# Kernel optimization log

Hardware: AMD Instinct MI355X
Metric: run time of the kernel (lower is better)

## Reference

```python
import jax, jax.numpy as jnp
import numpy as np

B, S, D, H = 4, 2048, 2048, 8192  # batch, seq, d_model, hidden (power of 2 for FHT)


def fwht(x):
    """Fast Walsh-Hadamard transform along the last axis, normalized by 1/sqrt(n).

    Iterative butterfly: O(n log n). n must be a power of 2.
    """
    orig_shape = x.shape
    n = orig_shape[-1]
    x = x.reshape(-1, n)
    h = 1
    while h < n:
        # view as (rows, n/(2h) blocks, 2 halves, h) and do the butterfly
        xb = x.reshape(-1, n // (2 * h), 2, h)
        a = xb[:, :, 0, :]
        b = xb[:, :, 1, :]
        x = jnp.stack([a + b, a - b], axis=2).reshape(-1, n)
        h *= 2
    scale = jnp.asarray(1.0 / np.sqrt(n), dtype=x.dtype)
    return (x * scale).reshape(orig_shape)


def setup_inputs() -> dict:
    key = jax.random.key(0)
    kx, k1, k2, k3 = jax.random.split(key, 4)
    x = jax.random.normal(kx, (B, S, D), dtype=jnp.float32)
    # nn.Linear weights: [out_features, in_features], no bias (Llama FFN style)
    W1 = jax.random.normal(k1, (H, D), dtype=jnp.float32) * (1.0 / np.sqrt(D))
    W2 = jax.random.normal(k2, (D, H), dtype=jnp.float32) * (1.0 / np.sqrt(H))
    W3 = jax.random.normal(k3, (H, D), dtype=jnp.float32) * (1.0 / np.sqrt(D))
    return {"x": x, "W1": W1, "W2": W2, "W3": W3}


def reference(x, W1, W2, W3):
    # w2( fht( silu(w1(x)) * w3(x) ) )
    up_gate = jnp.einsum("bsd,hd->bsh", x, W1)          # w1(x): [B,S,H]
    up_lin = jnp.einsum("bsd,hd->bsh", x, W3)           # w3(x): [B,S,H]
    hidden = jax.nn.silu(up_gate) * up_lin              # SwiGLU gate
    hidden = fwht(hidden)                               # fast Hadamard transform over H
    out = jnp.einsum("bsh,dh->bsd", hidden, W2)         # w2(.): [B,S,D]
    return out
```

## Files before the change

### kernel.cpp

```cpp
#include <hip/hip_runtime.h>

typedef __attribute__((ext_vector_type(8))) __bf16 bf16x8;
typedef __attribute__((ext_vector_type(4))) float f32x4;

#define GLOAD_LDS16(g, l)                                                     \
  __builtin_amdgcn_global_load_lds(                                           \
      (const __attribute__((address_space(1))) void*)(g),                     \
      (__attribute__((address_space(3))) void*)(l), 16, 0, 0)

#define BAR() __builtin_amdgcn_s_barrier()
#define SB0() __builtin_amdgcn_sched_barrier(0)
#define LGKM(n)                                                               \
  do {                                                                        \
    asm volatile("s_waitcnt lgkmcnt(" #n ")" ::: "memory");                   \
    SB0();                                                                    \
  } while (0)
#define VMCNT0() asm volatile("s_waitcnt vmcnt(0)" ::: "memory")
#define PRIO1() __builtin_amdgcn_s_setprio(1)
#define PRIO0() __builtin_amdgcn_s_setprio(0)
#define MFMA_BF16 __builtin_amdgcn_mfma_f32_16x16x32_bf16

__device__ __forceinline__ unsigned short f32_to_bf16(float f) {
  unsigned int u = __builtin_bit_cast(unsigned int, f);
  u += 0x7FFFu + ((u >> 16) & 1u);
  return (unsigned short)(u >> 16);
}

__global__ void conv_f32_bf16(const float* __restrict__ in,
                              unsigned short* __restrict__ out, int n4) {
  int stride = gridDim.x * blockDim.x;
  for (int i = blockIdx.x * blockDim.x + threadIdx.x; i < n4; i += stride) {
    float4 v = reinterpret_cast<const float4*>(in)[i];
    ushort4 o;
    o.x = f32_to_bf16(v.x);
    o.y = f32_to_bf16(v.y);
    o.z = f32_to_bf16(v.z);
    o.w = f32_to_bf16(v.w);
    reinterpret_cast<ushort4*>(out)[i] = o;
  }
}

__global__ void fwht_rows_bf16(const float* __restrict__ in,
                               unsigned short* __restrict__ out) {
  __shared__ float s[8192];
  const int tid = threadIdx.x;
  const float* row = in + (size_t)blockIdx.x * 8192;
#pragma unroll
  for (int i = 0; i < 8; ++i)
    reinterpret_cast<float4*>(s)[tid + i * 256] =
        reinterpret_cast<const float4*>(row)[tid + i * 256];
  for (int h = 1; h < 8192; h <<= 1) {
    __syncthreads();
#pragma unroll
    for (int it = 0; it < 16; ++it) {
      int i = tid + it * 256;
      int j = ((i & ~(h - 1)) << 1) | (i & (h - 1));
      float a = s[j], b = s[j + h];
      s[j] = a + b;
      s[j + h] = a - b;
    }
  }
  __syncthreads();
  const float scale = 0.011048543456039806f;
  unsigned short* orow = out + (size_t)blockIdx.x * 8192;
#pragma unroll
  for (int i = 0; i < 8; ++i) {
    float4 v = reinterpret_cast<const float4*>(s)[tid + i * 256];
    ushort4 o;
    o.x = f32_to_bf16(v.x * scale);
    o.y = f32_to_bf16(v.y * scale);
    o.z = f32_to_bf16(v.z * scale);
    o.w = f32_to_bf16(v.w * scale);
    reinterpret_cast<ushort4*>(orow)[tid + i * 256] = o;
  }
}

#define RD_A(arr, mi, bi)                                                     \
  arr[0] = *(const bf16x8*)(Lb + ((bi)*32768 + (mi)*2048) + rA0);             \
  arr[1] = *(const bf16x8*)(Lb + ((bi)*32768 + (mi)*2048) + rA1);
#define RD_B(arr, ni, bi)                                                     \
  arr[0] = *(const bf16x8*)(Lb + ((bi)*32768 + (ni)*2048) + rB0);             \
  arr[1] = *(const bf16x8*)(Lb + ((bi)*32768 + (ni)*2048) + rB1);

#define G2_TILE(bi, tt)                                                       \
  {                                                                           \
    if ((tt) + 1 < NT) {                                                      \
      unsigned short* dA = L + (((bi) ^ 1) * 16384) + wid * 512;              \
      unsigned short* dB = L + 32768 + (((bi) ^ 1) * 16384) + wid * 512;      \
      _Pragma("unroll") for (int i = 0; i < 4; ++i) {                         \
        GLOAD_LDS16(pA + i * s64, dA + i * 4096);                             \
        GLOAD_LDS16(pB + i * s64, dB + i * 4096);                             \
      }                                                                       \
    }                                                                         \
    SB0();                                                                    \
                                       \
    RD_A(ra[0], 0, bi) RD_A(ra[1], 1, bi)                                     \
    RD_B(rb[0], 0, bi) RD_B(rb[1], 1, bi)                                     \
    SB0();                                                                    \
                                                        \
    RD_A(ra[2], 2, bi) RD_A(ra[3], 3, bi)                                     \
    SB0();                                                                    \
    LGKM(4);                                                                  \
    PRIO1();                                                                  \
    _Pragma("unroll") for (int ks = 0; ks < 2; ++ks)                          \
        _Pragma("unroll") for (int m = 0; m < 2; ++m)                         \
            _Pragma("unroll") for (int n = 0; n < 2; ++n) acc[m][n] =         \
                MFMA_BF16(ra[m][ks], rb[n][ks], acc[m][n], 0, 0, 0);          \
    PRIO0();                                                                  \
    SB0();                                                                    \
                                                        \
    RD_B(rb[2], 2, bi) RD_B(rb[3], 3, bi)                                     \
    SB0();                                                                    \
    LGKM(4);                                                                  \
    PRIO1();                                                                  \
    _Pragma("unroll") for (int ks = 0; ks < 2; ++ks)                          \
        _Pragma("unroll") for (int m = 2; m < 4; ++m)                         \
            _Pragma("unroll") for (int n = 0; n < 2; ++n) acc[m][n] =         \
                MFMA_BF16(ra[m][ks], rb[n][ks], acc[m][n], 0, 0, 0);          \
    PRIO0();                                                                  \
    SB0();                                                                    \
                                                       \
    RD_A(ra2[0], 4, bi) RD_A(ra2[1], 5, bi)                                   \
    SB0();                                                                    \
    LGKM(4);                                                                  \
    PRIO1();                                                                  \
    _Pragma("unroll") for (int ks = 0; ks < 2; ++ks)                          \
        _Pragma("unroll") for (int m = 0; m < 4; ++m)                         \
            _Pragma("unroll") for (int n = 2; n < 4; ++n) acc[m][n] =         \
                MFMA_BF16(ra[m][ks], rb[n][ks], acc[m][n], 0, 0, 0);          \
    PRIO0();                                                                  \
    SB0();                                                                    \
                                                       \
    RD_A(ra2[2], 6, bi) RD_A(ra2[3], 7, bi)                                   \
    SB0();                                                                    \
    LGKM(4);                                                                  \
    PRIO1();                                                                  \
    _Pragma("unroll") for (int ks = 0; ks < 2; ++ks)                          \
        _Pragma("unroll") for (int m = 0; m < 2; ++m)                         \
            _Pragma("unroll") for (int n = 0; n < 4; ++n) acc[4 + m][n] =     \
                MFMA_BF16(ra2[m][ks], rb[n][ks], acc[4 + m][n], 0, 0, 0);     \
    PRIO0();                                                                  \
    SB0();                                                                    \
    LGKM(0);                                                                  \
    PRIO1();                                                                  \
    _Pragma("unroll") for (int ks = 0; ks < 2; ++ks)                          \
        _Pragma("unroll") for (int m = 2; m < 4; ++m)                         \
            _Pragma("unroll") for (int n = 0; n < 4; ++n) acc[4 + m][n] =     \
                MFMA_BF16(ra2[m][ks], rb[n][ks], acc[4 + m][n], 0, 0, 0);     \
    PRIO0();                                                                  \
    VMCNT0();                                                                 \
    BAR();                                                                    \
    pA += 128;                                                                \
    pB += 128;                                                                \
  }

__launch_bounds__(512, 2)
__global__ void gemm2_pipe(const unsigned short* __restrict__ A,
                           const unsigned short* __restrict__ Bt,
                           float* __restrict__ C, int M, int N, int K) {
  __shared__ __align__(16) unsigned short L[65536];
  const int tid = threadIdx.x, lane = tid & 63, wid = tid >> 6;
  const int wr = wid >> 2, wc = wid & 3;
  const int nbx = N >> 8;
  const int cpx = (int)gridDim.x >> 3;
  const int swz = ((int)blockIdx.x & 7) * cpx + ((int)blockIdx.x >> 3);
  const int bm = (swz / nbx) << 8, bn = (swz % nbx) << 8;
  const int NT = K >> 6;

  const int lp0 = (lane & 15) * 128 + (((lane >> 4) << 4) ^ ((lane & 7) << 4));
  const int lp1 =
      (lane & 15) * 128 + ((64 | ((lane >> 4) << 4)) ^ ((lane & 7) << 4));
  const int rA0 = wr * 16384 + lp0, rA1 = wr * 16384 + lp1;
  const int rB0 = 65536 + wc * 8192 + lp0, rB1 = 65536 + wc * 8192 + lp1;

  const int swzc = ((lane & 7) ^ (lane >> 3)) << 4;
  const char* pA = (const char*)A +
                   ((size_t)(bm + (wid << 3) + (lane >> 3)) * K) * 2 + swzc;
  const char* pB = (const char*)Bt +
                   ((size_t)(bn + (wid << 3) + (lane >> 3)) * K) * 2 + swzc;
  const size_t s64 = (size_t)K * 128;
  const char* Lb = (const char*)L;

  {
    unsigned short* dA = L + wid * 512;
    unsigned short* dB = L + 32768 + wid * 512;
#pragma unroll
    for (int i = 0; i < 4; ++i) {
      GLOAD_LDS16(pA + i * s64, dA + i * 4096);
      GLOAD_LDS16(pB + i * s64, dB + i * 4096);
    }
  }
  pA += 128;
  pB += 128;

  f32x4 acc[8][4];
#pragma unroll
  for (int m = 0; m < 8; ++m)
#pragma unroll
    for (int n = 0; n < 4; ++n) acc[m][n] = (f32x4)0.0f;
  bf16x8 ra[4][2], ra2[4][2], rb[4][2];

  VMCNT0();
  BAR();

  for (int t = 0; t < NT; t += 2) {
    G2_TILE(0, t)
    G2_TILE(1, t + 1)
  }

  const int er = (lane >> 4) << 2;
  const int ec = lane & 15;
#pragma unroll
  for (int mi = 0; mi < 8; ++mi)
#pragma unroll
    for (int n = 0; n < 4; ++n)
#pragma unroll
      for (int r = 0; r < 4; ++r) {
        size_t row = (size_t)(bm + wr * 128 + mi * 16 + er + r);
        size_t col = (size_t)(bn + wc * 64 + n * 16 + ec);
        C[row * N + col] = acc[mi][n][r];
      }
}

#define RD_A1(arr, mi, bi)                                                    \
  arr[0] = *(const bf16x8*)(Lb + ((bi)*32768 + (mi)*2048) + rA0);             \
  arr[1] = *(const bf16x8*)(Lb + ((bi)*32768 + (mi)*2048) + rA1);
#define RD_B1(arr, ni, bi)                                                    \
  arr[0] = *(const bf16x8*)(Lb + (65536 + (bi)*16384 + (ni)*2048) + rBp0);    \
  arr[1] = *(const bf16x8*)(Lb + (65536 + (bi)*16384 + (ni)*2048) + rBp1);
#define RD_B3(arr, ni, bi)                                                    \
  arr[0] = *(const bf16x8*)(Lb + (98304 + (bi)*16384 + (ni)*2048) + rBp0);    \
  arr[1] = *(const bf16x8*)(Lb + (98304 + (bi)*16384 + (ni)*2048) + rBp1);

#define G1_TILE(bi, tt)                                                       \
  {                                                                           \
    if ((tt) + 1 < NT) {                                                      \
      unsigned short* dA = L + (((bi) ^ 1) * 16384) + wid * 512;              \
      unsigned short* dB1 = L + 32768 + (((bi) ^ 1) * 8192) + wid * 512;      \
      unsigned short* dB3 = L + 49152 + (((bi) ^ 1) * 8192) + wid * 512;      \
      _Pragma("unroll") for (int i = 0; i < 4; ++i)                           \
          GLOAD_LDS16(pA + i * s64, dA + i * 4096);                           \
      _Pragma("unroll") for (int i = 0; i < 2; ++i) {                         \
        GLOAD_LDS16(pB1 + i * s64, dB1 + i * 4096);                           \
        GLOAD_LDS16(pB3 + i * s64, dB3 + i * 4096);                           \
      }                                                                       \
    }                                                                         \
    SB0();                                                                    \
                                      \
    RD_A1(ra[0], 0, bi) RD_A1(ra[1], 1, bi)                                   \
    RD_B1(rb1[0], 0, bi) RD_B1(rb1[1], 1, bi)                                 \
    SB0();                                                                    \
                                                        \
    RD_A1(ra[2], 2, bi) RD_A1(ra[3], 3, bi)                                   \
    SB0();                                                                    \
    LGKM(4);                                                                  \
    PRIO1();                                                                  \
    _Pragma("unroll") for (int ks = 0; ks < 2; ++ks)                          \
        _Pragma("unroll") for (int m = 0; m < 2; ++m)                         \
            _Pragma("unroll") for (int n = 0; n < 2; ++n) accG[m][n] =        \
                MFMA_BF16(ra[m][ks], rb1[n][ks], accG[m][n], 0, 0, 0);        \
    PRIO0();                                                                  \
    SB0();                                                                    \
                                                       \
    RD_B1(rb1[2], 2, bi) RD_B1(rb1[3], 3, bi)                                 \
    SB0();                                                                    \
    LGKM(4);                                                                  \
    PRIO1();                                                                  \
    _Pragma("unroll") for (int ks = 0; ks < 2; ++ks)                          \
        _Pragma("unroll") for (int m = 2; m < 4; ++m)                         \
            _Pragma("unroll") for (int n = 0; n < 2; ++n) accG[m][n] =        \
                MFMA_BF16(ra[m][ks], rb1[n][ks], accG[m][n], 0, 0, 0);        \
    PRIO0();                                                                  \
    SB0();                                                                    \
                                                       \
    RD_B3(rb3[2], 2, bi) RD_B3(rb3[3], 3, bi)                                 \
    SB0();                                                                    \
    LGKM(4);                                                                  \
    PRIO1();                                                                  \
    _Pragma("unroll") for (int ks = 0; ks < 2; ++ks)                          \
        _Pragma("unroll") for (int m = 0; m < 4; ++m)                         \
            _Pragma("unroll") for (int n = 2; n < 4; ++n) accG[m][n] =        \
                MFMA_BF16(ra[m][ks], rb1[n][ks], accG[m][n], 0, 0, 0);        \
    PRIO0();                                                                  \
    SB0();                                                                    \
                                                       \
    RD_B3(rb3[0], 0, bi) RD_B3(rb3[1], 1, bi)                                 \
    SB0();                                                                    \
    LGKM(4);                                                                  \
    PRIO1();                                                                  \
    _Pragma("unroll") for (int ks = 0; ks < 2; ++ks)                          \
        _Pragma("unroll") for (int m = 0; m < 4; ++m)                         \
            _Pragma("unroll") for (int n = 2; n < 4; ++n) accL[m][n] =        \
                MFMA_BF16(ra[m][ks], rb3[n][ks], accL[m][n], 0, 0, 0);        \
    PRIO0();                                                                  \
    SB0();                                                                    \
    LGKM(0);                                                                  \
    PRIO1();                                                                  \
    _Pragma("unroll") for (int ks = 0; ks < 2; ++ks)                          \
        _Pragma("unroll") for (int m = 0; m < 4; ++m)                         \
            _Pragma("unroll") for (int n = 0; n < 2; ++n) accL[m][n] =        \
                MFMA_BF16(ra[m][ks], rb3[n][ks], accL[m][n], 0, 0, 0);        \
    PRIO0();                                                                  \
    VMCNT0();                                                                 \
    BAR();                                                                    \
    pA += 128;                                                                \
    pB1 += 128;                                                               \
    pB3 += 128;                                                               \
  }

__launch_bounds__(512, 2)
__global__ void gemm1_pipe(const unsigned short* __restrict__ A,
                           const unsigned short* __restrict__ B1p,
                           const unsigned short* __restrict__ B3p,
                           unsigned short* __restrict__ Hout, int M, int N,
                           int K) {
  __shared__ __align__(16) unsigned short L[65536];
  const int tid = threadIdx.x, lane = tid & 63, wid = tid >> 6;
  const int wr = wid >> 1, wc = wid & 1;
  const int nby = M >> 8;
  const int cpx = (int)gridDim.x >> 3;
  const int swz = ((int)blockIdx.x & 7) * cpx + ((int)blockIdx.x >> 3);
  const int bm = (swz % nby) << 8;
  const int bn = (swz / nby) << 7;
  const int NT = K >> 6;

  const int lp0 = (lane & 15) * 128 + (((lane >> 4) << 4) ^ ((lane & 7) << 4));
  const int lp1 =
      (lane & 15) * 128 + ((64 | ((lane >> 4) << 4)) ^ ((lane & 7) << 4));
  const int rA0 = wr * 8192 + lp0, rA1 = wr * 8192 + lp1;
  const int rBp0 = wc * 8192 + lp0, rBp1 = wc * 8192 + lp1;

  const int swzc = ((lane & 7) ^ (lane >> 3)) << 4;
  const char* pA = (const char*)A +
                   ((size_t)(bm + (wid << 3) + (lane >> 3)) * K) * 2 + swzc;
  const char* pB1 = (const char*)B1p +
                    ((size_t)(bn + (wid << 3) + (lane >> 3)) * K) * 2 + swzc;
  const char* pB3 = (const char*)B3p +
                    ((size_t)(bn + (wid << 3) + (lane >> 3)) * K) * 2 + swzc;
  const size_t s64 = (size_t)K * 128;
  const char* Lb = (const char*)L;

  {
    unsigned short* dA = L + wid * 512;
    unsigned short* dB1 = L + 32768 + wid * 512;
    unsigned short* dB3 = L + 49152 + wid * 512;
#pragma unroll
    for (int i = 0; i < 4; ++i) GLOAD_LDS16(pA + i * s64, dA + i * 4096);
#pragma unroll
    for (int i = 0; i < 2; ++i) {
      GLOAD_LDS16(pB1 + i * s64, dB1 + i * 4096);
      GLOAD_LDS16(pB3 + i * s64, dB3 + i * 4096);
    }
  }
  pA += 128;
  pB1 += 128;
  pB3 += 128;

  f32x4 accG[4][4], accL[4][4];
#pragma unroll
  for (int m = 0; m < 4; ++m)
#pragma unroll
    for (int n = 0; n < 4; ++n) {
      accG[m][n] = (f32x4)0.0f;
      accL[m][n] = (f32x4)0.0f;
    }
  bf16x8 ra[4][2], rb1[4][2], rb3[4][2];

  VMCNT0();
  BAR();

  for (int t = 0; t < NT; t += 2) {
    G1_TILE(0, t)
    G1_TILE(1, t + 1)
  }

  const int er = (lane >> 4) << 2;
  const int ec = lane & 15;
#pragma unroll
  for (int m = 0; m < 4; ++m)
#pragma unroll
    for (int n = 0; n < 4; ++n)
#pragma unroll
      for (int r = 0; r < 4; ++r) {
        float g = accG[m][n][r];
        float li = accL[m][n][r];
        float h = (g / (1.0f + __expf(-g))) * li;
        size_t row = (size_t)(bm + wr * 64 + m * 16 + er + r);
        size_t col = (size_t)(bn + wc * 64 + n * 16 + ec);
        Hout[row * N + col] = f32_to_bf16(h);
      }
}

extern "C" void kernel_launch(void* const* d_in, const int* in_sizes, int n_in,
                              void* d_out, int out_size, void* d_ws,
                              size_t ws_size, hipStream_t stream) {
  const float* x = (const float*)d_in[0];
  const float* W1 = (const float*)d_in[1];
  const float* W2 = (const float*)d_in[2];
  const float* W3 = (const float*)d_in[3];
  float* out = (float*)d_out;

  const int M = 8192, D = 2048, H = 8192;
  const size_t NE = (size_t)16777216;

  unsigned short* xb = (unsigned short*)d_ws;
  unsigned short* w1b = xb + NE;
  unsigned short* w3b = w1b + NE;
  unsigned short* w2f = w3b + NE;
  unsigned short* hid = w2f + NE;

  conv_f32_bf16<<<2048, 256, 0, stream>>>(x, xb, (int)(NE / 4));
  conv_f32_bf16<<<2048, 256, 0, stream>>>(W1, w1b, (int)(NE / 4));
  conv_f32_bf16<<<2048, 256, 0, stream>>>(W3, w3b, (int)(NE / 4));
  fwht_rows_bf16<<<2048, 256, 0, stream>>>(W2, w2f);

  gemm1_pipe<<<(M / 256) * (H / 128), 512, 0, stream>>>(xb, w1b, w3b, hid, M,
                                                        H, D);
  gemm2_pipe<<<(M / 256) * (D / 256), 512, 0, stream>>>(hid, w2f, out, M, D,
                                                        H);
}
```

Before: 812.7 us.

## Load B operands directly from global into registers, keep only A in LDS

Both GEMMs now stage only the A tile through LDS. Each wave loads its B-operand fragments straight from global memory into double-buffered registers one tile ahead, and waits with a partial vmcnt. The warp layout changes to 2x4 waves, each covering 128 rows of A, which halves LDS use and removes the LDS write/read traffic for B. The cost is more VGPR pressure, uncoalesced 16-byte global loads of B with no sharing across waves, and more exposed global latency.

After: 1.086 ms. 1.34x slower.

```diff
diff --git a/kernel.cpp b/kernel.cpp
--- a/kernel.cpp
+++ b/kernel.cpp
@@ -15,7 +15,7 @@
     asm volatile("s_waitcnt lgkmcnt(" #n ")" ::: "memory");                   \
     SB0();                                                                    \
   } while (0)
-#define VMCNT0() asm volatile("s_waitcnt vmcnt(0)" ::: "memory")
+#define VMCNT(n) asm volatile("s_waitcnt vmcnt(" #n ")" ::: "memory")
 #define PRIO1() __builtin_amdgcn_s_setprio(1)
 #define PRIO0() __builtin_amdgcn_s_setprio(0)
 #define MFMA_BF16 __builtin_amdgcn_mfma_f32_16x16x32_bf16
@@ -75,90 +75,80 @@
   }
 }
 
-#define RD_A(arr, mi, bi)                                                     \
-  arr[0] = *(const bf16x8*)(Lb + ((bi)*32768 + (mi)*2048) + rA0);             \
-  arr[1] = *(const bf16x8*)(Lb + ((bi)*32768 + (mi)*2048) + rA1);
-#define RD_B(arr, ni, bi)                                                     \
-  arr[0] = *(const bf16x8*)(Lb + ((bi)*32768 + (ni)*2048) + rB0);             \
-  arr[1] = *(const bf16x8*)(Lb + ((bi)*32768 + (ni)*2048) + rB1);
-
-#define G2_TILE(bi, tt)                                                       \
+#define RDA(arr2, mi, bi)                                                     \
+  arr2[0] = *(const bf16x8*)(Lb + ((bi)*32768 + (mi)*2048) + rA0);            \
+  arr2[1] = *(const bf16x8*)(Lb + ((bi)*32768 + (mi)*2048) + rA1);
+
+#define LDB2(dst, nn, kss)                                                    \
+  dst = *(const bf16x8*)(pBr + (size_t)(nn)*262144 + (kss)*64);
+
+#define G2_BODY(bi, cur, nxt, tt)                                             \
   {                                                                           \
+    VMCNT(8);                \
+    BAR();                                                                    \
     if ((tt) + 1 < NT) {                                                      \
       unsigned short* dA = L + (((bi) ^ 1) * 16384) + wid * 512;              \
-      unsigned short* dB = L + 32768 + (((bi) ^ 1) * 16384) + wid * 512;      \
-      _Pragma("unroll") for (int i = 0; i < 4; ++i) {                         \
-        GLOAD_LDS16(pA + i * s64, dA + i * 4096);                             \
-        GLOAD_LDS16(pB + i * s64, dB + i * 4096);                             \
-      }                                                                       \
-    }                                                                         \
-    SB0();                                                                    \
-                                       \
-    RD_A(ra[0], 0, bi) RD_A(ra[1], 1, bi)                                     \
-    RD_B(rb[0], 0, bi) RD_B(rb[1], 1, bi)                                     \
-    SB0();                                                                    \
-                                                        \
-    RD_A(ra[2], 2, bi) RD_A(ra[3], 3, bi)                                     \
-    SB0();                                                                    \
-    LGKM(4);                                                                  \
-    PRIO1();                                                                  \
-    _Pragma("unroll") for (int ks = 0; ks < 2; ++ks)                          \
-        _Pragma("unroll") for (int m = 0; m < 2; ++m)                         \
-            _Pragma("unroll") for (int n = 0; n < 2; ++n) acc[m][n] =         \
-                MFMA_BF16(ra[m][ks], rb[n][ks], acc[m][n], 0, 0, 0);          \
-    PRIO0();                                                                  \
-    SB0();                                                                    \
-                                                        \
-    RD_B(rb[2], 2, bi) RD_B(rb[3], 3, bi)                                     \
-    SB0();                                                                    \
-    LGKM(4);                                                                  \
-    PRIO1();                                                                  \
-    _Pragma("unroll") for (int ks = 0; ks < 2; ++ks)                          \
-        _Pragma("unroll") for (int m = 2; m < 4; ++m)                         \
-            _Pragma("unroll") for (int n = 0; n < 2; ++n) acc[m][n] =         \
-                MFMA_BF16(ra[m][ks], rb[n][ks], acc[m][n], 0, 0, 0);          \
-    PRIO0();                                                                  \
-    SB0();                                                                    \
-                                                       \
-    RD_A(ra2[0], 4, bi) RD_A(ra2[1], 5, bi)                                   \
-    SB0();                                                                    \
-    LGKM(4);                                                                  \
-    PRIO1();                                                                  \
-    _Pragma("unroll") for (int ks = 0; ks < 2; ++ks)                          \
-        _Pragma("unroll") for (int m = 0; m < 4; ++m)                         \
-            _Pragma("unroll") for (int n = 2; n < 4; ++n) acc[m][n] =         \
-                MFMA_BF16(ra[m][ks], rb[n][ks], acc[m][n], 0, 0, 0);          \
-    PRIO0();                                                                  \
-    SB0();                                                                    \
-                                                       \
-    RD_A(ra2[2], 6, bi) RD_A(ra2[3], 7, bi)                                   \
-    SB0();                                                                    \
-    LGKM(4);                                                                  \
-    PRIO1();                                                                  \
-    _Pragma("unroll") for (int ks = 0; ks < 2; ++ks)                          \
-        _Pragma("unroll") for (int m = 0; m < 2; ++m)                         \
-            _Pragma("unroll") for (int n = 0; n < 4; ++n) acc[4 + m][n] =     \
-                MFMA_BF16(ra2[m][ks], rb[n][ks], acc[4 + m][n], 0, 0, 0);     \
+      _Pragma("unroll") for (int i = 0; i < 4; ++i)                           \
+          GLOAD_LDS16(pA + i * s64, dA + i * 4096);                           \
+    }                                                                         \
+    SB0();                                                                    \
+    if ((tt) + 1 < NT) {                                                      \
+      LDB2(nxt[0][0], 0, 0) LDB2(nxt[0][1], 0, 1)                             \
+      LDB2(nxt[1][0], 1, 0) LDB2(nxt[1][1], 1, 1)                             \
+    }                                                                         \
+    SB0();                                                                    \
+    RDA(raX[0], 0, bi) RDA(raX[1], 1, bi)                                     \
+    RDA(raY[0], 2, bi) RDA(raY[1], 3, bi)                                     \
+    SB0();                                                                    \
+    LGKM(4);                                                                  \
+    PRIO1();                                                                  \
+    _Pragma("unroll") for (int ks = 0; ks < 2; ++ks)                          \
+        _Pragma("unroll") for (int j = 0; j < 2; ++j)                         \
+            _Pragma("unroll") for (int n = 0; n < 4; ++n) acc[j][n] =         \
+                MFMA_BF16(raX[j][ks], cur[n][ks], acc[j][n], 0, 0, 0);        \
+    PRIO0();                                                                  \
+    SB0();                                                                    \
+    RDA(raX[0], 4, bi) RDA(raX[1], 5, bi)                                     \
+    SB0();                                                                    \
+    LGKM(4);                                                                  \
+    PRIO1();                                                                  \
+    _Pragma("unroll") for (int ks = 0; ks < 2; ++ks)                          \
+        _Pragma("unroll") for (int j = 0; j < 2; ++j)                         \
+            _Pragma("unroll") for (int n = 0; n < 4; ++n) acc[2 + j][n] =     \
+                MFMA_BF16(raY[j][ks], cur[n][ks], acc[2 + j][n], 0, 0, 0);    \
+    PRIO0();                                                                  \
+    SB0();                                                                    \
+    RDA(raY[0], 6, bi) RDA(raY[1], 7, bi)                                     \
+    SB0();                                                                    \
+    if ((tt) + 1 < NT) {                                                      \
+      LDB2(nxt[2][0], 2, 0) LDB2(nxt[2][1], 2, 1)                             \
+      LDB2(nxt[3][0], 3, 0) LDB2(nxt[3][1], 3, 1)                             \
+    }                                                                         \
+    SB0();                                                                    \
+    LGKM(4);                                                                  \
+    PRIO1();                                                                  \
+    _Pragma("unroll") for (int ks = 0; ks < 2; ++ks)                          \
+        _Pragma("unroll") for (int j = 0; j < 2; ++j)                         \
+            _Pragma("unroll") for (int n = 0; n < 4; ++n) acc[4 + j][n] =     \
+                MFMA_BF16(raX[j][ks], cur[n][ks], acc[4 + j][n], 0, 0, 0);    \
     PRIO0();                                                                  \
     SB0();                                                                    \
     LGKM(0);                                                                  \
     PRIO1();                                                                  \
     _Pragma("unroll") for (int ks = 0; ks < 2; ++ks)                          \
-        _Pragma("unroll") for (int m = 2; m < 4; ++m)                         \
-            _Pragma("unroll") for (int n = 0; n < 4; ++n) acc[4 + m][n] =     \
-                MFMA_BF16(ra2[m][ks], rb[n][ks], acc[4 + m][n], 0, 0, 0);     \
-    PRIO0();                                                                  \
-    VMCNT0();                                                                 \
-    BAR();                                                                    \
+        _Pragma("unroll") for (int j = 0; j < 2; ++j)                         \
+            _Pragma("unroll") for (int n = 0; n < 4; ++n) acc[6 + j][n] =     \
+                MFMA_BF16(raY[j][ks], cur[n][ks], acc[6 + j][n], 0, 0, 0);    \
+    PRIO0();                                                                  \
     pA += 128;                                                                \
-    pB += 128;                                                                \
+    pBr += 128;                                                               \
   }
 
 __launch_bounds__(512, 2)
-__global__ void gemm2_pipe(const unsigned short* __restrict__ A,
+__global__ void gemm2_dreg(const unsigned short* __restrict__ A,
                            const unsigned short* __restrict__ Bt,
                            float* __restrict__ C, int M, int N, int K) {
-  __shared__ __align__(16) unsigned short L[65536];
+  __shared__ __align__(16) unsigned short L[32768];
   const int tid = threadIdx.x, lane = tid & 63, wid = tid >> 6;
   const int wr = wid >> 2, wc = wid & 3;
   const int nbx = N >> 8;
@@ -171,41 +161,44 @@
   const int lp1 =
       (lane & 15) * 128 + ((64 | ((lane >> 4) << 4)) ^ ((lane & 7) << 4));
   const int rA0 = wr * 16384 + lp0, rA1 = wr * 16384 + lp1;
-  const int rB0 = 65536 + wc * 8192 + lp0, rB1 = 65536 + wc * 8192 + lp1;
 
   const int swzc = ((lane & 7) ^ (lane >> 3)) << 4;
   const char* pA = (const char*)A +
                    ((size_t)(bm + (wid << 3) + (lane >> 3)) * K) * 2 + swzc;
-  const char* pB = (const char*)Bt +
-                   ((size_t)(bn + (wid << 3) + (lane >> 3)) * K) * 2 + swzc;
   const size_t s64 = (size_t)K * 128;
   const char* Lb = (const char*)L;
 
+  const char* pBr =
+      (const char*)Bt +
+      ((size_t)(bn + wc * 64 + (lane & 15)) * K + ((lane >> 4) << 3)) * 2;
+
   {
     unsigned short* dA = L + wid * 512;
-    unsigned short* dB = L + 32768 + wid * 512;
-#pragma unroll
-    for (int i = 0; i < 4; ++i) {
-      GLOAD_LDS16(pA + i * s64, dA + i * 4096);
-      GLOAD_LDS16(pB + i * s64, dB + i * 4096);
-    }
-  }
+#pragma unroll
+    for (int i = 0; i < 4; ++i) GLOAD_LDS16(pA + i * s64, dA + i * 4096);
+  }
+  SB0();
+  bf16x8 rbA[4][2], rbB[4][2];
+  {
+    LDB2(rbA[0][0], 0, 0) LDB2(rbA[0][1], 0, 1)
+    LDB2(rbA[1][0], 1, 0) LDB2(rbA[1][1], 1, 1)
+    LDB2(rbA[2][0], 2, 0) LDB2(rbA[2][1], 2, 1)
+    LDB2(rbA[3][0], 3, 0) LDB2(rbA[3][1], 3, 1)
+  }
+  SB0();
   pA += 128;
-  pB += 128;
+  pBr += 128;
 
   f32x4 acc[8][4];
 #pragma unroll
   for (int m = 0; m < 8; ++m)
 #pragma unroll
     for (int n = 0; n < 4; ++n) acc[m][n] = (f32x4)0.0f;
-  bf16x8 ra[4][2], ra2[4][2], rb[4][2];
-
-  VMCNT0();
-  BAR();
+  bf16x8 raX[2][2], raY[2][2];
 
   for (int t = 0; t < NT; t += 2) {
-    G2_TILE(0, t)
-    G2_TILE(1, t + 1)
+    G2_BODY(0, rbA, rbB, t)
+    G2_BODY(1, rbB, rbA, t + 1)
   }
 
   const int er = (lane >> 4) << 2;
@@ -222,101 +215,95 @@
       }
 }
 
-#define RD_A1(arr, mi, bi)                                                    \
-  arr[0] = *(const bf16x8*)(Lb + ((bi)*32768 + (mi)*2048) + rA0);             \
-  arr[1] = *(const bf16x8*)(Lb + ((bi)*32768 + (mi)*2048) + rA1);
-#define RD_B1(arr, ni, bi)                                                    \
-  arr[0] = *(const bf16x8*)(Lb + (65536 + (bi)*16384 + (ni)*2048) + rBp0);    \
-  arr[1] = *(const bf16x8*)(Lb + (65536 + (bi)*16384 + (ni)*2048) + rBp1);
-#define RD_B3(arr, ni, bi)                                                    \
-  arr[0] = *(const bf16x8*)(Lb + (98304 + (bi)*16384 + (ni)*2048) + rBp0);    \
-  arr[1] = *(const bf16x8*)(Lb + (98304 + (bi)*16384 + (ni)*2048) + rBp1);
-
-#define G1_TILE(bi, tt)                                                       \
+#define LDB1(dst, base, nn, kss)                                              \
+  dst = *(const bf16x8*)(base + (size_t)(nn)*65536 + (kss)*64);
+
+#define G1_BODY(bi, c1, c3, x1, x3, tt)                                       \
   {                                                                           \
+    VMCNT(8);                                                                 \
+    BAR();                                                                    \
     if ((tt) + 1 < NT) {                                                      \
       unsigned short* dA = L + (((bi) ^ 1) * 16384) + wid * 512;              \
-      unsigned short* dB1 = L + 32768 + (((bi) ^ 1) * 8192) + wid * 512;      \
-      unsigned short* dB3 = L + 49152 + (((bi) ^ 1) * 8192) + wid * 512;      \
       _Pragma("unroll") for (int i = 0; i < 4; ++i)                           \
           GLOAD_LDS16(pA + i * s64, dA + i * 4096);                           \
-      _Pragma("unroll") for (int i = 0; i < 2; ++i) {                         \
-        GLOAD_LDS16(pB1 + i * s64, dB1 + i * 4096);                           \
-        GLOAD_LDS16(pB3 + i * s64, dB3 + i * 4096);                           \
-      }                                                                       \
-    }                                                                         \
-    SB0();                                                                    \
-                                      \
-    RD_A1(ra[0], 0, bi) RD_A1(ra[1], 1, bi)                                   \
-    RD_B1(rb1[0], 0, bi) RD_B1(rb1[1], 1, bi)                                 \
-    SB0();                                                                    \
-                                                        \
-    RD_A1(ra[2], 2, bi) RD_A1(ra[3], 3, bi)                                   \
-    SB0();                                                                    \
-    LGKM(4);                                                                  \
-    PRIO1();                                                                  \
-    _Pragma("unroll") for (int ks = 0; ks < 2; ++ks)                          \
-        _Pragma("unroll") for (int m = 0; m < 2; ++m)                         \
-            _Pragma("unroll") for (int n = 0; n < 2; ++n) accG[m][n] =        \
-                MFMA_BF16(ra[m][ks], rb1[n][ks], accG[m][n], 0, 0, 0);        \
-    PRIO0();                                                                  \
-    SB0();                                                                    \
-                                                       \
-    RD_B1(rb1[2], 2, bi) RD_B1(rb1[3], 3, bi)                                 \
-    SB0();                                                                    \
-    LGKM(4);                                                                  \
-    PRIO1();                                                                  \
-    _Pragma("unroll") for (int ks = 0; ks < 2; ++ks)                          \
-        _Pragma("unroll") for (int m = 2; m < 4; ++m)                         \
-            _Pragma("unroll") for (int n = 0; n < 2; ++n) accG[m][n] =        \
-                MFMA_BF16(ra[m][ks], rb1[n][ks], accG[m][n], 0, 0, 0);        \
-    PRIO0();                                                                  \
-    SB0();                                                                    \
-                                                       \
-    RD_B3(rb3[2], 2, bi) RD_B3(rb3[3], 3, bi)                                 \
-    SB0();                                                                    \
-    LGKM(4);                                                                  \
-    PRIO1();                                                                  \
-    _Pragma("unroll") for (int ks = 0; ks < 2; ++ks)                          \
-        _Pragma("unroll") for (int m = 0; m < 4; ++m)                         \
-            _Pragma("unroll") for (int n = 2; n < 4; ++n) accG[m][n] =        \
-                MFMA_BF16(ra[m][ks], rb1[n][ks], accG[m][n], 0, 0, 0);        \
-    PRIO0();                                                                  \
-    SB0();                                                                    \
-                                                       \
-    RD_B3(rb3[0], 0, bi) RD_B3(rb3[1], 1, bi)                                 \
-    SB0();                                                                    \
-    LGKM(4);                                                                  \
-    PRIO1();                                                                  \
-    _Pragma("unroll") for (int ks = 0; ks < 2; ++ks)                          \
-        _Pragma("unroll") for (int m = 0; m < 4; ++m)                         \
-            _Pragma("unroll") for (int n = 2; n < 4; ++n) accL[m][n] =        \
-                MFMA_BF16(ra[m][ks], rb3[n][ks], accL[m][n], 0, 0, 0);        \
+    }                                                                         \
+    SB0();                                                                    \
+    if ((tt) + 1 < NT) {                                                      \
+      LDB1(x1[0][0], pB1r, 0, 0) LDB1(x1[0][1], pB1r, 0, 1)                   \
+      LDB1(x1[1][0], pB1r, 1, 0) LDB1(x1[1][1], pB1r, 1, 1)                   \
+    }                                                                         \
+    SB0();                                                                    \
+    RDA(raX[0], 0, bi) RDA(raX[1], 1, bi)                                     \
+    RDA(raY[0], 2, bi) RDA(raY[1], 3, bi)                                     \
+    SB0();                                                                    \
+    LGKM(4);                                                                  \
+    PRIO1();                                                                  \
+    _Pragma("unroll") for (int ks = 0; ks < 2; ++ks)                          \
+        _Pragma("unroll") for (int j = 0; j < 2; ++j)                         \
+            _Pragma("unroll") for (int n = 0; n < 2; ++n) {                   \
+      accG[j][n] = MFMA_BF16(raX[j][ks], c1[n][ks], accG[j][n], 0, 0, 0);     \
+      accL[j][n] = MFMA_BF16(raX[j][ks], c3[n][ks], accL[j][n], 0, 0, 0);     \
+    }                                                                         \
+    PRIO0();                                                                  \
+    SB0();                                                                    \
+    RDA(raX[0], 4, bi) RDA(raX[1], 5, bi)                                     \
+    SB0();                                                                    \
+    LGKM(4);                                                                  \
+    PRIO1();                                                                  \
+    _Pragma("unroll") for (int ks = 0; ks < 2; ++ks)                          \
+        _Pragma("unroll") for (int j = 0; j < 2; ++j)                         \
+            _Pragma("unroll") for (int n = 0; n < 2; ++n) {                   \
+      accG[2 + j][n] = MFMA_BF16(raY[j][ks], c1[n][ks], accG[2 + j][n], 0,    \
+                                 0, 0);                                       \
+      accL[2 + j][n] = MFMA_BF16(raY[j][ks], c3[n][ks], accL[2 + j][n], 0,    \
+                                 0, 0);                                       \
+    }                                                                         \
+    PRIO0();                                                                  \
+    SB0();                                                                    \
+    RDA(raY[0], 6, bi) RDA(raY[1], 7, bi)                                     \
+    SB0();                                                                    \
+    if ((tt) + 1 < NT) {                                                      \
+      LDB1(x3[0][0], pB3r, 0, 0) LDB1(x3[0][1], pB3r, 0, 1)                   \
+      LDB1(x3[1][0], pB3r, 1, 0) LDB1(x3[1][1], pB3r, 1, 1)                   \
+    }                                                                         \
+    SB0();                                                                    \
+    LGKM(4);                                                                  \
+    PRIO1();                                                                  \
+    _Pragma("unroll") for (int ks = 0; ks < 2; ++ks)                          \
+        _Pragma("unroll") for (int j = 0; j < 2; ++j)                         \
+            _Pragma("unroll") for (int n = 0; n < 2; ++n) {                   \
+      accG[4 + j][n] = MFMA_BF16(raX[j][ks], c1[n][ks], accG[4 + j][n], 0,    \
+                                 0, 0);                                       \
+      accL[4 + j][n] = MFMA_BF16(raX[j][ks], c3[n][ks], accL[4 + j][n], 0,    \
+                                 0, 0);                                       \
+    }                                                                         \
     PRIO0();                                                                  \
     SB0();                                                                    \
     LGKM(0);                                                                  \
     PRIO1();                                                                  \
     _Pragma("unroll") for (int ks = 0; ks < 2; ++ks)                          \
-        _Pragma("unroll") for (int m = 0; m < 4; ++m)                         \
-            _Pragma("unroll") for (int n = 0; n < 2; ++n) accL[m][n] =        \
-                MFMA_BF16(ra[m][ks], rb3[n][ks], accL[m][n], 0, 0, 0);        \
-    PRIO0();                                                                  \
-    VMCNT0();                                                                 \
-    BAR();                                                                    \
+        _Pragma("unroll") for (int j = 0; j < 2; ++j)                         \
+            _Pragma("unroll") for (int n = 0; n < 2; ++n) {                   \
+      accG[6 + j][n] = MFMA_BF16(raY[j][ks], c1[n][ks], accG[6 + j][n], 0,    \
+                                 0, 0);                                       \
+      accL[6 + j][n] = MFMA_BF16(raY[j][ks], c3[n][ks], accL[6 + j][n], 0,    \
+                                 0, 0);                                       \
+    }                                                                         \
+    PRIO0();                                                                  \
     pA += 128;                                                                \
-    pB1 += 128;                                                               \
-    pB3 += 128;                                                               \
+    pB1r += 128;                                                              \
+    pB3r += 128;                                                              \
   }
 
 __launch_bounds__(512, 2)
-__global__ void gemm1_pipe(const unsigned short* __restrict__ A,
-                           const unsigned short* __restrict__ B1p,
-                           const unsigned short* __restrict__ B3p,
+__global__ void gemm1_dreg(const unsigned short* __restrict__ A,
+                           const unsigned short* __restrict__ B1,
+                           const unsigned short* __restrict__ B3,
                            unsigned short* __restrict__ Hout, int M, int N,
                            int K) {
-  __shared__ __align__(16) unsigned short L[65536];
+  __shared__ __align__(16) unsigned short L[32768];
   const int tid = threadIdx.x, lane = tid & 63, wid = tid >> 6;
-  const int wr = wid >> 1, wc = wid & 1;
+  const int wr = wid >> 2, wc = wid & 3;
   const int nby = M >> 8;
   const int cpx = (int)gridDim.x >> 3;
   const int swz = ((int)blockIdx.x & 7) * cpx + ((int)blockIdx.x >> 3);
@@ -327,66 +314,67 @@
   const int lp0 = (lane & 15) * 128 + (((lane >> 4) << 4) ^ ((lane & 7) << 4));
   const int lp1 =
       (lane & 15) * 128 + ((64 | ((lane >> 4) << 4)) ^ ((lane & 7) << 4));
-  const int rA0 = wr * 8192 + lp0, rA1 = wr * 8192 + lp1;
-  const int rBp0 = wc * 8192 + lp0, rBp1 = wc * 8192 + lp1;
+  const int rA0 = wr * 16384 + lp0, rA1 = wr * 16384 + lp1;
 
   const int swzc = ((lane & 7) ^ (lane >> 3)) << 4;
   const char* pA = (const char*)A +
                    ((size_t)(bm + (wid << 3) + (lane >> 3)) * K) * 2 + swzc;
-  const char* pB1 = (const char*)B1p +
-                    ((size_t)(bn + (wid << 3) + (lane >> 3)) * K) * 2 + swzc;
-  const char* pB3 = (const char*)B3p +
-                    ((size_t)(bn + (wid << 3) + (lane >> 3)) * K) * 2 + swzc;
   const size_t s64 = (size_t)K * 128;
   const char* Lb = (const char*)L;
 
+  const char* pB1r =
+      (const char*)B1 +
+      ((size_t)(bn + wc * 32 + (lane & 15)) * K + ((lane >> 4) << 3)) * 2;
+  const char* pB3r =
+      (const char*)B3 +
+      ((size_t)(bn + wc * 32 + (lane & 15)) * K + ((lane >> 4) << 3)) * 2;
+
   {
     unsigned short* dA = L + wid * 512;
-    unsigned short* dB1 = L + 32768 + wid * 512;
-    unsigned short* dB3 = L + 49152 + wid * 512;
 #pragma unroll
     for (int i = 0; i < 4; ++i) GLOAD_LDS16(pA + i * s64, dA + i * 4096);
-#pragma unroll
-    for (int i = 0; i < 2; ++i) {
-      GLOAD_LDS16(pB1 + i * s64, dB1 + i * 4096);
-      GLOAD_LDS16(pB3 + i * s64, dB3 + i * 4096);
-    }
-  }
+  }
+  SB0();
+  bf16x8 r1A[2][2], r1B[2][2], r3A[2][2], r3B[2][2];
+  {
+    LDB1(r1A[0][0], pB1r, 0, 0) LDB1(r1A[0][1], pB1r, 0, 1)
+    LDB1(r1A[1][0], pB1r, 1, 0) LDB1(r1A[1][1], pB1r, 1, 1)
+    LDB1(r3A[0][0], pB3r, 0, 0) LDB1(r3A[0][1], pB3r, 0, 1)
+    LDB1(r3A[1][0], pB3r, 1, 0) LDB1(r3A[1][1], pB3r, 1, 1)
+  }
+  SB0();
   pA += 128;
-  pB1 += 128;
-  pB3 += 128;
-
-  f32x4 accG[4][4], accL[4][4];
-#pragma unroll
-  for (int m = 0; m < 4; ++m)
-#pragma unroll
-    for (int n = 0; n < 4; ++n) {
+  pB1r += 128;
+  pB3r += 128;
+
+  f32x4 accG[8][2], accL[8][2];
+#pragma unroll
+  for (int m = 0; m < 8; ++m)
+#pragma unroll
+    for (int n = 0; n < 2; ++n) {
       accG[m][n] = (f32x4)0.0f;
       accL[m][n] = (f32x4)0.0f;
     }
-  bf16x8 ra[4][2], rb1[4][2], rb3[4][2];
-
-  VMCNT0();
-  BAR();
+  bf16x8 raX[2][2], raY[2][2];
 
   for (int t = 0; t < NT; t += 2) {
-    G1_TILE(0, t)
-    G1_TILE(1, t + 1)
+    G1_BODY(0, r1A, r3A, r1B, r3B, t)
+    G1_BODY(1, r1B, r3B, r1A, r3A, t + 1)
   }
 
   const int er = (lane >> 4) << 2;
   const int ec = lane & 15;
 #pragma unroll
-  for (int m = 0; m < 4; ++m)
-#pragma unroll
-    for (int n = 0; n < 4; ++n)
+  for (int mi = 0; mi < 8; ++mi)
+#pragma unroll
+    for (int n = 0; n < 2; ++n)
 #pragma unroll
       for (int r = 0; r < 4; ++r) {
-        float g = accG[m][n][r];
-        float li = accL[m][n][r];
+        float g = accG[mi][n][r];
+        float li = accL[mi][n][r];
         float h = (g / (1.0f + __expf(-g))) * li;
-        size_t row = (size_t)(bm + wr * 64 + m * 16 + er + r);
-        size_t col = (size_t)(bn + wc * 64 + n * 16 + ec);
+        size_t row = (size_t)(bm + wr * 128 + mi * 16 + er + r);
+        size_t col = (size_t)(bn + wc * 32 + n * 16 + ec);
         Hout[row * N + col] = f32_to_bf16(h);
       }
 }
@@ -414,8 +402,8 @@
   conv_f32_bf16<<<2048, 256, 0, stream>>>(W3, w3b, (int)(NE / 4));
   fwht_rows_bf16<<<2048, 256, 0, stream>>>(W2, w2f);
 
-  gemm1_pipe<<<(M / 256) * (H / 128), 512, 0, stream>>>(xb, w1b, w3b, hid, M,
+  gemm1_dreg<<<(M / 256) * (H / 128), 512, 0, stream>>>(xb, w1b, w3b, hid, M,
                                                         H, D);
-  gemm2_pipe<<<(M / 256) * (D / 256), 512, 0, stream>>>(hid, w2f, out, M, D,
+  gemm2_dreg<<<(M / 256) * (D / 256), 512, 0, stream>>>(hid, w2f, out, M, D,
                                                         H);
 }
```

## Rotate last MFMA chunk of each K-tile into next tile's LDS read phase

Applied to the files above, without the earlier changes.

Both GEMM main loops are restructured so the final group of MFMAs from one K-tile is deferred into the start of the next tile, where it overlaps the LDS fragment reads. A peeled epilogue after the loop issues the leftover MFMAs. LDS read grouping is also reorganized into fewer, larger batches with different register arrays. The intent is to hide LDS latency and shrink MFMA idle gaps. The cost is extra live registers across the barrier and more complex waitcnt reasoning.

Result: slower. 1.166 ms (+43.4%).

```diff
diff --git a/kernel.cpp b/kernel.cpp
--- a/kernel.cpp
+++ b/kernel.cpp
@@ -93,61 +93,59 @@
       }                                                                       \
     }                                                                         \
     SB0();                                                                    \
-                                       \
-    RD_A(ra[0], 0, bi) RD_A(ra[1], 1, bi)                                     \
+                 \
+    RD_A(ra_lo[0], 0, bi) RD_A(ra_lo[1], 1, bi)                               \
+    RD_A(ra_mi[0], 2, bi) RD_A(ra_mi[1], 3, bi)                               \
+    SB0();                                                                    \
+    if ((tt) > 0) {                 \
+      PRIO1();                                                                \
+      _Pragma("unroll") for (int ks = 0; ks < 2; ++ks)                        \
+          _Pragma("unroll") for (int j = 0; j < 2; ++j)                       \
+              _Pragma("unroll") for (int n = 0; n < 4; ++n) acc[6 + j][n] =   \
+                  MFMA_BF16(ra_67[j][ks], rb[n][ks], acc[6 + j][n], 0, 0, 0); \
+      PRIO0();                                                                \
+    }                                                                         \
+    SB0();                                                                    \
+                                                 \
     RD_B(rb[0], 0, bi) RD_B(rb[1], 1, bi)                                     \
-    SB0();                                                                    \
-                                                        \
-    RD_A(ra[2], 2, bi) RD_A(ra[3], 3, bi)                                     \
-    SB0();                                                                    \
-    LGKM(4);                                                                  \
+    RD_B(rb[2], 2, bi) RD_B(rb[3], 3, bi)                                     \
+    SB0();                                                                    \
+    LGKM(4);                          \
     PRIO1();                                                                  \
     _Pragma("unroll") for (int ks = 0; ks < 2; ++ks)                          \
-        _Pragma("unroll") for (int m = 0; m < 2; ++m)                         \
-            _Pragma("unroll") for (int n = 0; n < 2; ++n) acc[m][n] =         \
-                MFMA_BF16(ra[m][ks], rb[n][ks], acc[m][n], 0, 0, 0);          \
+        _Pragma("unroll") for (int j = 0; j < 2; ++j)                         \
+            _Pragma("unroll") for (int n = 0; n < 2; ++n) {                   \
+      acc[j][n] = MFMA_BF16(ra_lo[j][ks], rb[n][ks], acc[j][n], 0, 0, 0);     \
+      acc[2 + j][n] = MFMA_BF16(ra_mi[j][ks], rb[n][ks], acc[2 + j][n], 0,    \
+                                0, 0);                                        \
+    }                                                                         \
     PRIO0();                                                                  \
     SB0();                                                                    \
-                                                        \
-    RD_B(rb[2], 2, bi) RD_B(rb[3], 3, bi)                                     \
-    SB0();                                                                    \
-    LGKM(4);                                                                  \
+                                                               \
+    RD_A(ra_45[0], 4, bi) RD_A(ra_45[1], 5, bi)                               \
+    SB0();                                                                    \
+    LGKM(4);                                  \
     PRIO1();                                                                  \
     _Pragma("unroll") for (int ks = 0; ks < 2; ++ks)                          \
-        _Pragma("unroll") for (int m = 2; m < 4; ++m)                         \
-            _Pragma("unroll") for (int n = 0; n < 2; ++n) acc[m][n] =         \
-                MFMA_BF16(ra[m][ks], rb[n][ks], acc[m][n], 0, 0, 0);          \
+        _Pragma("unroll") for (int j = 0; j < 2; ++j)                         \
+            _Pragma("unroll") for (int n = 2; n < 4; ++n) {                   \
+      acc[j][n] = MFMA_BF16(ra_lo[j][ks], rb[n][ks], acc[j][n], 0, 0, 0);     \
+      acc[2 + j][n] = MFMA_BF16(ra_mi[j][ks], rb[n][ks], acc[2 + j][n], 0,    \
+                                0, 0);                                        \
+    }                                                                         \
     PRIO0();                                                                  \
     SB0();                                                                    \
-                                                       \
-    RD_A(ra2[0], 4, bi) RD_A(ra2[1], 5, bi)                                   \
-    SB0();                                                                    \
-    LGKM(4);                                                                  \
+                                    \
+    RD_A(ra_67[0], 6, bi) RD_A(ra_67[1], 7, bi)                               \
+    SB0();                                                                    \
+    LGKM(4);                                     \
     PRIO1();                                                                  \
     _Pragma("unroll") for (int ks = 0; ks < 2; ++ks)                          \
-        _Pragma("unroll") for (int m = 0; m < 4; ++m)                         \
-            _Pragma("unroll") for (int n = 2; n < 4; ++n) acc[m][n] =         \
-                MFMA_BF16(ra[m][ks], rb[n][ks], acc[m][n], 0, 0, 0);          \
+        _Pragma("unroll") for (int j = 0; j < 2; ++j)                         \
+            _Pragma("unroll") for (int n = 0; n < 4; ++n) acc[4 + j][n] =     \
+                MFMA_BF16(ra_45[j][ks], rb[n][ks], acc[4 + j][n], 0, 0, 0);   \
     PRIO0();                                                                  \
-    SB0();                                                                    \
-                                                       \
-    RD_A(ra2[2], 6, bi) RD_A(ra2[3], 7, bi)                                   \
-    SB0();                                                                    \
-    LGKM(4);                                                                  \
-    PRIO1();                                                                  \
-    _Pragma("unroll") for (int ks = 0; ks < 2; ++ks)                          \
-        _Pragma("unroll") for (int m = 0; m < 2; ++m)                         \
-            _Pragma("unroll") for (int n = 0; n < 4; ++n) acc[4 + m][n] =     \
-                MFMA_BF16(ra2[m][ks], rb[n][ks], acc[4 + m][n], 0, 0, 0);     \
-    PRIO0();                                                                  \
-    SB0();                                                                    \
-    LGKM(0);                                                                  \
-    PRIO1();                                                                  \
-    _Pragma("unroll") for (int ks = 0; ks < 2; ++ks)                          \
-        _Pragma("unroll") for (int m = 2; m < 4; ++m)                         \
-            _Pragma("unroll") for (int n = 0; n < 4; ++n) acc[4 + m][n] =     \
-                MFMA_BF16(ra2[m][ks], rb[n][ks], acc[4 + m][n], 0, 0, 0);     \
-    PRIO0();                                                                  \
+    LGKM(0);                                  \
     VMCNT0();                                                                 \
     BAR();                                                                    \
     pA += 128;                                                                \
@@ -155,9 +153,9 @@
   }
 
 __launch_bounds__(512, 2)
-__global__ void gemm2_pipe(const unsigned short* __restrict__ A,
-                           const unsigned short* __restrict__ Bt,
-                           float* __restrict__ C, int M, int N, int K) {
+__global__ void gemm2_rot(const unsigned short* __restrict__ A,
+                          const unsigned short* __restrict__ Bt,
+                          float* __restrict__ C, int M, int N, int K) {
   __shared__ __align__(16) unsigned short L[65536];
   const int tid = threadIdx.x, lane = tid & 63, wid = tid >> 6;
   const int wr = wid >> 2, wc = wid & 3;
@@ -198,7 +196,7 @@
   for (int m = 0; m < 8; ++m)
 #pragma unroll
     for (int n = 0; n < 4; ++n) acc[m][n] = (f32x4)0.0f;
-  bf16x8 ra[4][2], ra2[4][2], rb[4][2];
+  bf16x8 ra_lo[2][2], ra_mi[2][2], ra_45[2][2], ra_67[2][2], rb[4][2];
 
   VMCNT0();
   BAR();
@@ -207,6 +205,16 @@
     G2_TILE(0, t)
     G2_TILE(1, t + 1)
   }
+  PRIO1();
+#pragma unroll
+  for (int ks = 0; ks < 2; ++ks)
+#pragma unroll
+    for (int j = 0; j < 2; ++j)
+#pragma unroll
+      for (int n = 0; n < 4; ++n)
+        acc[6 + j][n] = MFMA_BF16(ra_67[j][ks], rb[n][ks], acc[6 + j][n], 0,
+                                  0, 0);
+  PRIO0();
 
   const int er = (lane >> 4) << 2;
   const int ec = lane & 15;
@@ -246,60 +254,43 @@
       }                                                                       \
     }                                                                         \
     SB0();                                                                    \
-                                      \
+            \
+    RD_B1(rb1[0], 0, bi) RD_B1(rb1[1], 1, bi)                                 \
+    RD_B1(rb1[2], 2, bi) RD_B1(rb1[3], 3, bi)                                 \
+    SB0();                                                                    \
+    if ((tt) > 0) {    \
+      PRIO1();                                                                \
+      _Pragma("unroll") for (int ks = 0; ks < 2; ++ks)                        \
+          _Pragma("unroll") for (int m = 0; m < 4; ++m)                       \
+              _Pragma("unroll") for (int n = 0; n < 2; ++n)                   \
+                  accL[m][2 + n] = MFMA_BF16(ra[m][ks], rb3hi[n][ks],         \
+                                             accL[m][2 + n], 0, 0, 0);        \
+      PRIO0();                                                                \
+    }                                                                         \
+    SB0();                                                                    \
+                                   \
     RD_A1(ra[0], 0, bi) RD_A1(ra[1], 1, bi)                                   \
-    RD_B1(rb1[0], 0, bi) RD_B1(rb1[1], 1, bi)                                 \
-    SB0();                                                                    \
-                                                        \
     RD_A1(ra[2], 2, bi) RD_A1(ra[3], 3, bi)                                   \
     SB0();                                                                    \
-    LGKM(4);                                                                  \
-    PRIO1();                                                                  \
-    _Pragma("unroll") for (int ks = 0; ks < 2; ++ks)                          \
-        _Pragma("unroll") for (int m = 0; m < 2; ++m)                         \
-            _Pragma("unroll") for (int n = 0; n < 2; ++n) accG[m][n] =        \
-                MFMA_BF16(ra[m][ks], rb1[n][ks], accG[m][n], 0, 0, 0);        \
-    PRIO0();                                                                  \
-    SB0();                                                                    \
-                                                       \
-    RD_B1(rb1[2], 2, bi) RD_B1(rb1[3], 3, bi)                                 \
-    SB0();                                                                    \
-    LGKM(4);                                                                  \
-    PRIO1();                                                                  \
-    _Pragma("unroll") for (int ks = 0; ks < 2; ++ks)                          \
-        _Pragma("unroll") for (int m = 2; m < 4; ++m)                         \
-            _Pragma("unroll") for (int n = 0; n < 2; ++n) accG[m][n] =        \
-                MFMA_BF16(ra[m][ks], rb1[n][ks], accG[m][n], 0, 0, 0);        \
-    PRIO0();                                                                  \
-    SB0();                                                                    \
-                                                       \
-    RD_B3(rb3[2], 2, bi) RD_B3(rb3[3], 3, bi)                                 \
-    SB0();                                                                    \
-    LGKM(4);                                                                  \
+    RD_B3(rb3hi[0], 2, bi) RD_B3(rb3hi[1], 3, bi)                             \
+    SB0();                                                                    \
+    LGKM(4);                                  \
     PRIO1();                                                                  \
     _Pragma("unroll") for (int ks = 0; ks < 2; ++ks)                          \
         _Pragma("unroll") for (int m = 0; m < 4; ++m)                         \
-            _Pragma("unroll") for (int n = 2; n < 4; ++n) accG[m][n] =        \
+            _Pragma("unroll") for (int n = 0; n < 4; ++n) accG[m][n] =        \
                 MFMA_BF16(ra[m][ks], rb1[n][ks], accG[m][n], 0, 0, 0);        \
     PRIO0();                                                                  \
     SB0();                                                                    \
-                                                       \
-    RD_B3(rb3[0], 0, bi) RD_B3(rb3[1], 1, bi)                                 \
-    SB0();                                                                    \
-    LGKM(4);                                                                  \
-    PRIO1();                                                                  \
-    _Pragma("unroll") for (int ks = 0; ks < 2; ++ks)                          \
-        _Pragma("unroll") for (int m = 0; m < 4; ++m)                         \
-            _Pragma("unroll") for (int n = 2; n < 4; ++n) accL[m][n] =        \
-                MFMA_BF16(ra[m][ks], rb3[n][ks], accL[m][n], 0, 0, 0);        \
-    PRIO0();                                                                  \
-    SB0();                                                                    \
-    LGKM(0);                                                                  \
+                                                          \
+    RD_B3(rb3lo[0], 0, bi) RD_B3(rb3lo[1], 1, bi)                             \
+    SB0();                                                                    \
+    LGKM(0);                                            \
     PRIO1();                                                                  \
     _Pragma("unroll") for (int ks = 0; ks < 2; ++ks)                          \
         _Pragma("unroll") for (int m = 0; m < 4; ++m)                         \
             _Pragma("unroll") for (int n = 0; n < 2; ++n) accL[m][n] =        \
-                MFMA_BF16(ra[m][ks], rb3[n][ks], accL[m][n], 0, 0, 0);        \
+                MFMA_BF16(ra[m][ks], rb3lo[n][ks], accL[m][n], 0, 0, 0);      \
     PRIO0();                                                                  \
     VMCNT0();                                                                 \
     BAR();                                                                    \
@@ -309,11 +300,11 @@
   }
 
 __launch_bounds__(512, 2)
-__global__ void gemm1_pipe(const unsigned short* __restrict__ A,
-                           const unsigned short* __restrict__ B1p,
-                           const unsigned short* __restrict__ B3p,
-                           unsigned short* __restrict__ Hout, int M, int N,
-                           int K) {
+__global__ void gemm1_rot(const unsigned short* __restrict__ A,
+                          const unsigned short* __restrict__ B1p,
+                          const unsigned short* __restrict__ B3p,
+                          unsigned short* __restrict__ Hout, int M, int N,
+                          int K) {
   __shared__ __align__(16) unsigned short L[65536];
   const int tid = threadIdx.x, lane = tid & 63, wid = tid >> 6;
   const int wr = wid >> 1, wc = wid & 1;
@@ -364,7 +355,7 @@
       accG[m][n] = (f32x4)0.0f;
       accL[m][n] = (f32x4)0.0f;
     }
-  bf16x8 ra[4][2], rb1[4][2], rb3[4][2];
+  bf16x8 ra[4][2], rb1[4][2], rb3hi[2][2], rb3lo[2][2];
 
   VMCNT0();
   BAR();
@@ -373,6 +364,16 @@
     G1_TILE(0, t)
     G1_TILE(1, t + 1)
   }
+  PRIO1();
+#pragma unroll
+  for (int ks = 0; ks < 2; ++ks)
+#pragma unroll
+    for (int m = 0; m < 4; ++m)
+#pragma unroll
+      for (int n = 0; n < 2; ++n)
+        accL[m][2 + n] =
+            MFMA_BF16(ra[m][ks], rb3hi[n][ks], accL[m][2 + n], 0, 0, 0);
+  PRIO0();
 
   const int er = (lane >> 4) << 2;
   const int ec = lane & 15;
@@ -414,8 +415,8 @@
   conv_f32_bf16<<<2048, 256, 0, stream>>>(W3, w3b, (int)(NE / 4));
   fwht_rows_bf16<<<2048, 256, 0, stream>>>(W2, w2f);
 
-  gemm1_pipe<<<(M / 256) * (H / 128), 512, 0, stream>>>(xb, w1b, w3b, hid, M,
-                                                        H, D);
-  gemm2_pipe<<<(M / 256) * (D / 256), 512, 0, stream>>>(hid, w2f, out, M, D,
-                                                        H);
-}
+  gemm1_rot<<<(M / 256) * (H / 128), 512, 0, stream>>>(xb, w1b, w3b, hid, M,
+                                                       H, D);
+  gemm2_rot<<<(M / 256) * (D / 256), 512, 0, stream>>>(hid, w2f, out, M, D,
+                                                       H);
+}
```
